# Kernel optimization log

Measured on AMD Instinct MI355X. Metric: run time of the kernel, lower is better.

The kernel has to match this reference:

```python
import jax, jax.numpy as jnp
import numpy as np

N = 100000      # nodes
E = 1600000     # edges (before self-loops)
IN_C = 128
HID = 256
L = 4
EPS = 1e-5


def setup_inputs() -> dict:
    key = jax.random.key(0)
    ks = jax.random.split(key, 12)
    s = 0.05
    x = jax.random.normal(ks[0], (N, IN_C), dtype=jnp.float32)
    edge_index = jax.random.randint(ks[1], (2, E), 0, N, dtype=jnp.int64)
    enc_w = jax.random.normal(ks[2], (IN_C, HID), dtype=jnp.float32) * s
    enc_b = jnp.zeros((HID,), jnp.float32)
    conv_w = jax.random.normal(ks[3], (L, HID, HID), dtype=jnp.float32) * s
    conv_b = jnp.zeros((L, HID), jnp.float32)
    ln_g = jnp.ones((L, HID), jnp.float32)
    ln_b = jnp.zeros((L, HID), jnp.float32)
    lin1_w = jax.random.normal(ks[4], (HID, HID // 2), dtype=jnp.float32) * s
    lin1_b = jnp.zeros((HID // 2,), jnp.float32)
    lin2_w = jax.random.normal(ks[5], (HID // 2, 1), dtype=jnp.float32) * s
    lin2_b = jnp.zeros((1,), jnp.float32)
    return dict(x=x, edge_index=edge_index, enc_w=enc_w, enc_b=enc_b,
                conv_w=conv_w, conv_b=conv_b, ln_g=ln_g, ln_b=ln_b,
                lin1_w=lin1_w, lin1_b=lin1_b, lin2_w=lin2_w, lin2_b=lin2_b)


def _layer_norm(h, g, b):
    mu = jnp.mean(h, axis=-1, keepdims=True)
    var = jnp.mean(jnp.square(h - mu), axis=-1, keepdims=True)
    return (h - mu) * jax.lax.rsqrt(var + EPS) * g + b


def reference(x, edge_index, enc_w, enc_b, conv_w, conv_b, ln_g, ln_b,
              lin1_w, lin1_b, lin2_w, lin2_b):
    loops = jnp.arange(N, dtype=edge_index.dtype)
    row = jnp.concatenate([edge_index[0], loops])   # source
    col = jnp.concatenate([edge_index[1], loops])   # target
    # GCN symmetric norm with self-loop weight 1 (improved=False)
    deg = jax.ops.segment_sum(jnp.ones(row.shape[0], jnp.float32), col,
                              num_segments=N)
    dis = jnp.where(deg > 0, jax.lax.rsqrt(deg), 0.0)  # deg^-1/2, [N]

    h = x @ enc_w + enc_b
    for i in range(L):
        hw = h @ conv_w[i]
        # norm_e = dis[row]*dis[col]: scale at source, aggregate, scale at target
        agg = jax.ops.segment_sum((hw * dis[:, None])[row], col,
                                  num_segments=N)
        h = agg * dis[:, None] + conv_b[i]
        h = jax.nn.relu(_layer_norm(h, ln_g[i], ln_b[i]))
        # dropout p=0.1 is identity in eval mode
    h = jax.nn.relu(h @ lin1_w + lin1_b)
    return h @ lin2_w + lin2_b  # [N, 1]
```

## Files before the change

### kernel.cpp

```cpp
#include <hip/hip_runtime.h>

#define N_NODES 100000
#define N_EDGES 1600000
#define IN_C    128
#define HID     256
#define NLAYER  4

#define NBUCK 391
#define BCAP  8192
#define EPB   4096
#define CAPL  6144

typedef __attribute__((ext_vector_type(8))) __bf16 bf16x8;
typedef __attribute__((ext_vector_type(4))) float  floatx4;
typedef __attribute__((ext_vector_type(2))) float  floatx2;

__device__ inline unsigned short f2b(float f) {
    unsigned u = __builtin_bit_cast(unsigned, f);
    return (unsigned short)((u + 0x7fffu + ((u >> 16) & 1u)) >> 16);
}
__device__ inline void acc8p(floatx2* a, uint4 v) {
    unsigned wds[4] = {v.x, v.y, v.z, v.w};
    #pragma unroll
    for (int k = 0; k < 4; ++k) {
        floatx2 t;
        t.x = __builtin_bit_cast(float, wds[k] << 16);
        t.y = __builtin_bit_cast(float, wds[k] & 0xffff0000u);
        a[k] += t;
    }
}

__global__ void kb_zero(int* g, int m) {
    int i = blockIdx.x * blockDim.x + threadIdx.x;
    if (i < m) g[i] = 0;
}

__global__ __launch_bounds__(256) void kb_scatter(
        const int* __restrict__ row, const int* __restrict__ col,
        int* __restrict__ gfill, uint2* __restrict__ pairs, int e) {
    __shared__ uint2 ep[EPB];
    __shared__ int hist[NBUCK];
    __shared__ int lbase[NBUCK];
    const int tid  = threadIdx.x;
    const int base = blockIdx.x * EPB;
    for (int b = tid; b < NBUCK; b += 256) hist[b] = 0;
    __syncthreads();
    #pragma unroll
    for (int k = 0; k < EPB / 256; ++k) {
        int i = base + k * 256 + tid;
        uint2 pr = make_uint2(0xffffffffu, 0u);
        if (i < e) {
            pr.x = (unsigned)col[i];
            pr.y = (unsigned)row[i];
            atomicAdd(&hist[pr.x >> 8], 1);
        }
        ep[k * 256 + tid] = pr;
    }
    __syncthreads();
    for (int b = tid; b < NBUCK; b += 256) {
        int h = hist[b];
        lbase[b] = h ? atomicAdd(&gfill[b], h) : 0;
    }
    __syncthreads();
    for (int b = tid; b < NBUCK; b += 256) hist[b] = 0;
    __syncthreads();
    #pragma unroll
    for (int k = 0; k < EPB / 256; ++k) {
        uint2 pr = ep[k * 256 + tid];
        if (pr.x != 0xffffffffu) {
            int bk = pr.x >> 8;
            int p  = lbase[bk] + atomicAdd(&hist[bk], 1);
            if (p < BCAP) pairs[(size_t)bk * BCAP + p] = pr;
        }
    }
}

__global__ void kb_scan(const int* __restrict__ gfill, int* __restrict__ boff,
                        int* __restrict__ offs) {
    __shared__ int wsum[8];
    const int t = threadIdx.x, lane = t & 63, w = t >> 6;
    int v = (t < NBUCK) ? gfill[t] : 0;
    int inc = v;
    #pragma unroll
    for (int o = 1; o < 64; o <<= 1) { int u = __shfl_up(inc, o); if (lane >= o) inc += u; }
    if (lane == 63) wsum[w] = inc;
    __syncthreads();
    if (t == 0) { int r = 0; for (int i = 0; i < 8; ++i) { int x = wsum[i]; wsum[i] = r; r += x; } }
    __syncthreads();
    int excl = wsum[w] + inc - v;
    if (t <= NBUCK) boff[t] = excl;
    if (t == 0) offs[N_NODES] = N_EDGES;
}

__global__ __launch_bounds__(256) void kb_build(
        const uint2* __restrict__ pairs, const int* __restrict__ gfill,
        const int* __restrict__ boff,
        int* __restrict__ offs, float* __restrict__ dis,
        int* __restrict__ srcl, int n) {
    __shared__ int lcnt[256];
    __shared__ int lstart[256];
    __shared__ int wsum[4];
    __shared__ int sl[CAPL];
    const int b = blockIdx.x;
    const int tid = threadIdx.x, lane = tid & 63, w = tid >> 6;
    int cnt = gfill[b]; if (cnt > CAPL) cnt = CAPL;
    const int base = boff[b];
    const uint2* bp = pairs + (size_t)b * BCAP;
    lcnt[tid] = 0;
    __syncthreads();
    for (int i = tid; i < cnt; i += 256)
        atomicAdd(&lcnt[bp[i].x & 255], 1);
    __syncthreads();
    int v = lcnt[tid];
    int inc = v;
    #pragma unroll
    for (int o = 1; o < 64; o <<= 1) { int u = __shfl_up(inc, o); if (lane >= o) inc += u; }
    if (lane == 63) wsum[w] = inc;
    __syncthreads();
    if (tid == 0) { int r = 0; for (int i = 0; i < 4; ++i) { int x = wsum[i]; wsum[i] = r; r += x; } }
    __syncthreads();
    int excl = wsum[w] + inc - v;
    lstart[tid] = excl;
    int node = (b << 8) + tid;
    if (node < n) {
        dis[node]  = rsqrtf((float)(v + 1));
        offs[node] = base + excl;
    }
    __syncthreads();
    lcnt[tid] = 0;
    __syncthreads();
    for (int i = tid; i < cnt; i += 256) {
        uint2 pr = bp[i];
        int c = pr.x & 255;
        int q = lstart[c] + atomicAdd(&lcnt[c], 1);
        sl[q] = (int)pr.y;
    }
    __syncthreads();
    for (int i = tid; i < cnt; i += 256)
        srcl[base + i] = sl[i];
}

__global__ void k_wt_all(const float* __restrict__ enc_w, const float* __restrict__ conv_w,
                         const float* __restrict__ w1,
                         unsigned short* __restrict__ enc_t, unsigned short* __restrict__ conv_t,
                         unsigned short* __restrict__ lin1_t) {
    int idx = blockIdx.x * blockDim.x + threadIdx.x;
    if (idx < IN_C * HID) {
        int k = idx / HID, n = idx % HID;
        enc_t[n * IN_C + k] = f2b(enc_w[idx]);
    } else if (idx < IN_C * HID + NLAYER * HID * HID) {
        int r = idx - IN_C * HID;
        int l = r / (HID * HID);
        int e = r % (HID * HID);
        int k = e / HID, n = e % HID;
        conv_t[(size_t)l * HID * HID + n * HID + k] = f2b(conv_w[r]);
    } else if (idx < IN_C * HID + NLAYER * HID * HID + HID * (HID / 2)) {
        int e = idx - (IN_C * HID + NLAYER * HID * HID);
        int k = e / (HID / 2), n = e % (HID / 2);
        lin1_t[n * HID + k] = f2b(w1[e]);
    }
}

template<int MODE>
__global__ __launch_bounds__(256) void k_mm(
        const void* __restrict__ Ain,
        const unsigned short* __restrict__ Wt,
        const float* __restrict__ bias, const float* __restrict__ scale,
        void* __restrict__ Cout, int M, int K, int Nn) {
    __shared__ unsigned short As[128 * 32];
    __shared__ unsigned short Bs[128 * 32];
    const int tid  = threadIdx.x;
    const int lane = tid & 63;
    const int w    = tid >> 6;
    const int bm   = blockIdx.x * 128;
    const int bn   = blockIdx.y * 128;

    const int i0 = tid, i1 = tid + 256;
    const int r0 = i0 >> 2, r1 = i1 >> 2;
    const int q0 = i0 & 3,  q1 = i1 & 3;
    const int a_off0 = min(bm + r0, M - 1) * K + q0 * 8;
    const int a_off1 = min(bm + r1, M - 1) * K + q1 * 8;
    const int b_off0 = (bn + r0) * K + q0 * 8;
    const int b_off1 = (bn + r1) * K + q1 * 8;

    floatx4 acc[4][4];
    #pragma unroll
    for (int i = 0; i < 4; ++i)
        #pragma unroll
        for (int j = 0; j < 4; ++j)
            acc[i][j] = (floatx4){0.f, 0.f, 0.f, 0.f};

    const int wm = (w & 1) * 64;
    const int wn = (w >> 1) * 64;
    const int fm = lane & 15;
    const int fq = (lane >> 4) * 8;

    const unsigned short* Ab = (const unsigned short*)Ain;
    const float*          Af = (const float*)Ain;

    uint4 ra0, ra1, rb0, rb1;
    auto loadA = [&](int koff, uint4& oa0, uint4& oa1) {
        if (MODE == 0) {
            float4 f0 = *(const float4*)(Af + a_off0 + koff);
            float4 f1 = *(const float4*)(Af + a_off0 + koff + 4);
            oa0.x = (unsigned)f2b(f0.x) | ((unsigned)f2b(f0.y) << 16);
            oa0.y = (unsigned)f2b(f0.z) | ((unsigned)f2b(f0.w) << 16);
            oa0.z = (unsigned)f2b(f1.x) | ((unsigned)f2b(f1.y) << 16);
            oa0.w = (unsigned)f2b(f1.z) | ((unsigned)f2b(f1.w) << 16);
            float4 g0 = *(const float4*)(Af + a_off1 + koff);
            float4 g1 = *(const float4*)(Af + a_off1 + koff + 4);
            oa1.x = (unsigned)f2b(g0.x) | ((unsigned)f2b(g0.y) << 16);
            oa1.y = (unsigned)f2b(g0.z) | ((unsigned)f2b(g0.w) << 16);
            oa1.z = (unsigned)f2b(g1.x) | ((unsigned)f2b(g1.y) << 16);
            oa1.w = (unsigned)f2b(g1.z) | ((unsigned)f2b(g1.w) << 16);
        } else {
            oa0 = *(const uint4*)(Ab + a_off0 + koff);
            oa1 = *(const uint4*)(Ab + a_off1 + koff);
        }
    };

    loadA(0, ra0, ra1);
    rb0 = *(const uint4*)(Wt + b_off0);
    rb1 = *(const uint4*)(Wt + b_off1);

    const int KT = K >> 5;
    for (int kt = 0; kt < KT; ++kt) {
        ((uint4*)As)[i0] = ra0; ((uint4*)As)[i1] = ra1;
        ((uint4*)Bs)[i0] = rb0; ((uint4*)Bs)[i1] = rb1;
        __syncthreads();
        if (kt + 1 < KT) {
            int k0 = (kt + 1) << 5;
            loadA(k0, ra0, ra1);
            rb0 = *(const uint4*)(Wt + b_off0 + k0);
            rb1 = *(const uint4*)(Wt + b_off1 + k0);
        }
        bf16x8 af[4], bfr[4];
        #pragma unroll
        for (int i = 0; i < 4; ++i)
            af[i] = *(const bf16x8*)(const void*)(As + (wm + i * 16 + fm) * 32 + fq);
        #pragma unroll
        for (int j = 0; j < 4; ++j)
            bfr[j] = *(const bf16x8*)(const void*)(Bs + (wn + j * 16 + fm) * 32 + fq);
        #pragma unroll
        for (int i = 0; i < 4; ++i)
            #pragma unroll
            for (int j = 0; j < 4; ++j)
                acc[i][j] = __builtin_amdgcn_mfma_f32_16x16x32_bf16(af[i], bfr[j], acc[i][j], 0, 0, 0);
        __syncthreads();
    }

    const int quad = lane >> 4;
    #pragma unroll
    for (int i = 0; i < 4; ++i) {
        #pragma unroll
        for (int r = 0; r < 4; ++r) {
            int row = bm + wm + i * 16 + quad * 4 + r;
            if (row >= M) continue;
            float sc = scale ? scale[row] : 1.f;
            #pragma unroll
            for (int j = 0; j < 4; ++j) {
                int colg = bn + wn + j * 16 + fm;
                float v = acc[i][j][r];
                if (MODE == 0) v += bias[colg];
                v *= sc;
                ((unsigned short*)Cout)[(size_t)row * Nn + colg] = f2b(v);
            }
        }
    }
}

__global__ __launch_bounds__(256) void k_head(
        const unsigned short* __restrict__ A,
        const unsigned short* __restrict__ Wt,
        const float* __restrict__ b1, const float* __restrict__ w2,
        const float* __restrict__ b2, float* __restrict__ out, int M) {
    const int K = 256;
    __shared__ unsigned short As[128 * 32];
    __shared__ unsigned short Bs[128 * 32];
    const int tid  = threadIdx.x;
    const int lane = tid & 63;
    const int w    = tid >> 6;
    const int bm   = blockIdx.x * 128;

    const int i0 = tid, i1 = tid + 256;
    const int r0 = i0 >> 2, r1 = i1 >> 2;
    const int q0 = i0 & 3,  q1 = i1 & 3;
    const int a_off0 = min(bm + r0, M - 1) * K + q0 * 8;
    const int a_off1 = min(bm + r1, M - 1) * K + q1 * 8;
    const int b_off0 = r0 * K + q0 * 8;
    const int b_off1 = r1 * K + q1 * 8;

    uint4 ra0, ra1, rb0, rb1;
    floatx4 acc[4][4];
    #pragma unroll
    for (int i = 0; i < 4; ++i)
        #pragma unroll
        for (int j = 0; j < 4; ++j)
            acc[i][j] = (floatx4){0.f, 0.f, 0.f, 0.f};

    const int wm = (w & 1) * 64;
    const int wn = (w >> 1) * 64;
    const int fm = lane & 15;
    const int fq = (lane >> 4) * 8;

    ra0 = *(const uint4*)(A + a_off0);
    ra1 = *(const uint4*)(A + a_off1);
    rb0 = *(const uint4*)(Wt + b_off0);
    rb1 = *(const uint4*)(Wt + b_off1);

    for (int kt = 0; kt < 8; ++kt) {
        ((uint4*)As)[i0] = ra0; ((uint4*)As)[i1] = ra1;
        ((uint4*)Bs)[i0] = rb0; ((uint4*)Bs)[i1] = rb1;
        __syncthreads();
        if (kt + 1 < 8) {
            int k0 = (kt + 1) << 5;
            ra0 = *(const uint4*)(A + a_off0 + k0);
            ra1 = *(const uint4*)(A + a_off1 + k0);
            rb0 = *(const uint4*)(Wt + b_off0 + k0);
            rb1 = *(const uint4*)(Wt + b_off1 + k0);
        }
        bf16x8 af[4], bfr[4];
        #pragma unroll
        for (int i = 0; i < 4; ++i)
            af[i] = *(const bf16x8*)(const void*)(As + (wm + i * 16 + fm) * 32 + fq);
        #pragma unroll
        for (int j = 0; j < 4; ++j)
            bfr[j] = *(const bf16x8*)(const void*)(Bs + (wn + j * 16 + fm) * 32 + fq);
        #pragma unroll
        for (int i = 0; i < 4; ++i)
            #pragma unroll
            for (int j = 0; j < 4; ++j)
                acc[i][j] = __builtin_amdgcn_mfma_f32_16x16x32_bf16(af[i], bfr[j], acc[i][j], 0, 0, 0);
        __syncthreads();
    }

    float* red = (float*)As;
    const int q = lane >> 4;
    float b1v[4], w2v[4];
    #pragma unroll
    for (int j = 0; j < 4; ++j) {
        int col = wn + j * 16 + fm;
        b1v[j] = b1[col]; w2v[j] = w2[col];
    }
    #pragma unroll
    for (int i = 0; i < 4; ++i) {
        #pragma unroll
        for (int r = 0; r < 4; ++r) {
            float s = 0.f;
            #pragma unroll
            for (int j = 0; j < 4; ++j)
                s += fmaxf(acc[i][j][r] + b1v[j], 0.f) * w2v[j];
            #pragma unroll
            for (int off = 1; off < 16; off <<= 1) s += __shfl_xor(s, off);
            if (fm == 0) {
                int m = wm + i * 16 + q * 4 + r;
                red[m * 2 + (wn >> 6)] = s;
            }
        }
    }
    __syncthreads();
    if (tid < 128) {
        int row = bm + tid;
        if (row < M) out[row] = red[tid * 2] + red[tid * 2 + 1] + b2[0];
    }
}

__global__ void k_agg(const unsigned short* __restrict__ hw, const int* __restrict__ srcl,
                      const int* __restrict__ offs, const float* __restrict__ dis,
                      const float* __restrict__ cb, const float* __restrict__ g,
                      const float* __restrict__ bt, unsigned short* __restrict__ hout, int n) {
    int gtid = blockIdx.x * blockDim.x + threadIdx.x;
    int node = __builtin_amdgcn_readfirstlane(gtid >> 6);
    int lane = threadIdx.x & 63;
    const int half = lane >> 5;
    const int sub  = lane & 31;
    const uint4* T = (const uint4*)hw;

    floatx2 A0[4], C0[4];
    #pragma unroll
    for (int k = 0; k < 4; ++k) { A0[k] = (floatx2){0.f, 0.f}; C0[k] = (floatx2){0.f, 0.f}; }
    if (half == 0) {
        uint4 v = T[(size_t)node * 32 + sub];
        acc8p(A0, v);
    }
    int p = offs[node], pe = offs[node + 1];
    for (; p + 15 < pe; p += 16) {
        int s[16];
        #pragma unroll
        for (int t = 0; t < 16; ++t) s[t] = srcl[p + t];
        uint4 v0 = T[(size_t)(half ? s[1]  : s[0])  * 32 + sub];
        uint4 v1 = T[(size_t)(half ? s[3]  : s[2])  * 32 + sub];
        uint4 v2 = T[(size_t)(half ? s[5]  : s[4])  * 32 + sub];
        uint4 v3 = T[(size_t)(half ? s[7]  : s[6])  * 32 + sub];
        uint4 v4 = T[(size_t)(half ? s[9]  : s[8])  * 32 + sub];
        uint4 v5 = T[(size_t)(half ? s[11] : s[10]) * 32 + sub];
        uint4 v6 = T[(size_t)(half ? s[13] : s[12]) * 32 + sub];
        uint4 v7 = T[(size_t)(half ? s[15] : s[14]) * 32 + sub];
        acc8p(A0, v0); acc8p(C0, v1); acc8p(A0, v2); acc8p(C0, v3);
        acc8p(A0, v4); acc8p(C0, v5); acc8p(A0, v6); acc8p(C0, v7);
    }
    for (; p + 7 < pe; p += 8) {
        int s0 = srcl[p],     s1 = srcl[p + 1], s2 = srcl[p + 2], s3 = srcl[p + 3];
        int s4 = srcl[p + 4], s5 = srcl[p + 5], s6 = srcl[p + 6], s7 = srcl[p + 7];
        uint4 v0 = T[(size_t)(half ? s1 : s0) * 32 + sub];
        uint4 v1 = T[(size_t)(half ? s3 : s2) * 32 + sub];
        uint4 v2 = T[(size_t)(half ? s5 : s4) * 32 + sub];
        uint4 v3 = T[(size_t)(half ? s7 : s6) * 32 + sub];
        acc8p(A0, v0); acc8p(C0, v1); acc8p(A0, v2); acc8p(C0, v3);
    }
    for (; p + 1 < pe; p += 2) {
        int s0 = srcl[p], s1 = srcl[p + 1];
        uint4 v = T[(size_t)(half ? s1 : s0) * 32 + sub];
        acc8p(A0, v);
    }
    if (p < pe && half == 0) {
        uint4 v = T[(size_t)srcl[p] * 32 + sub];
        acc8p(A0, v);
    }
    float a[8];
    #pragma unroll
    for (int k = 0; k < 4; ++k) {
        floatx2 t = A0[k] + C0[k];
        a[2 * k]     = t.x + __shfl_xor(t.x, 32);
        a[2 * k + 1] = t.y + __shfl_xor(t.y, 32);
    }
    float dc = dis[node];
    const float4* cb4 = (const float4*)cb;
    const float4* g4  = (const float4*)g;
    const float4* bt4 = (const float4*)bt;
    float4 cba = cb4[sub * 2], cbb = cb4[sub * 2 + 1];
    float h[8];
    h[0] = fmaf(a[0], dc, cba.x); h[1] = fmaf(a[1], dc, cba.y);
    h[2] = fmaf(a[2], dc, cba.z); h[3] = fmaf(a[3], dc, cba.w);
    h[4] = fmaf(a[4], dc, cbb.x); h[5] = fmaf(a[5], dc, cbb.y);
    h[6] = fmaf(a[6], dc, cbb.z); h[7] = fmaf(a[7], dc, cbb.w);
    float s = 0.f, sq = 0.f;
    #pragma unroll
    for (int j = 0; j < 8; ++j) { s += h[j]; sq += h[j] * h[j]; }
    #pragma unroll
    for (int off = 1; off < 32; off <<= 1) { s += __shfl_xor(s, off); sq += __shfl_xor(sq, off); }
    float mu  = s * (1.f / 256.f);
    float var = sq * (1.f / 256.f) - mu * mu;
    float inv = rsqrtf(var + 1e-5f);
    if (half == 0) {
        float4 ga = g4[sub * 2], gb = g4[sub * 2 + 1];
        float4 ba = bt4[sub * 2], bb = bt4[sub * 2 + 1];
        float gv[8] = {ga.x, ga.y, ga.z, ga.w, gb.x, gb.y, gb.z, gb.w};
        float bv[8] = {ba.x, ba.y, ba.z, ba.w, bb.x, bb.y, bb.z, bb.w};
        unsigned short o[8];
        #pragma unroll
        for (int j = 0; j < 8; ++j)
            o[j] = f2b(fmaxf(fmaf((h[j] - mu) * inv, gv[j], bv[j]), 0.f));
        uint4 st;
        st.x = (unsigned)o[0] | ((unsigned)o[1] << 16);
        st.y = (unsigned)o[2] | ((unsigned)o[3] << 16);
        st.z = (unsigned)o[4] | ((unsigned)o[5] << 16);
        st.w = (unsigned)o[6] | ((unsigned)o[7] << 16);
        ((uint4*)hout)[(size_t)node * 32 + sub] = st;
    }
}

extern "C" void kernel_launch(void* const* d_in, const int* in_sizes, int n_in,
                              void* d_out, int out_size, void* d_ws, size_t ws_size,
                              hipStream_t stream) {
    const float* x      = (const float*)d_in[0];
    const int*   ei     = (const int*)d_in[1];
    const float* enc_w  = (const float*)d_in[2];
    const float* enc_b  = (const float*)d_in[3];
    const float* conv_w = (const float*)d_in[4];
    const float* conv_b = (const float*)d_in[5];
    const float* ln_g   = (const float*)d_in[6];
    const float* ln_b   = (const float*)d_in[7];
    const float* w1     = (const float*)d_in[8];
    const float* b1     = (const float*)d_in[9];
    const float* w2     = (const float*)d_in[10];
    const float* b2     = (const float*)d_in[11];
    float* out = (float*)d_out;

    char* ws = (char*)d_ws;
    size_t off = 0;
    auto alloc = [&](size_t bytes) -> void* {
        void* p = ws + off;
        off = (off + bytes + 255) & ~(size_t)255;
        return p;
    };
    int*   offs  = (int*)alloc((size_t)(N_NODES + 1) * 4);
    int*   srcl  = (int*)alloc((size_t)N_EDGES * 4);
    float* dis   = (float*)alloc((size_t)N_NODES * 4);
    int*   gfill = (int*)alloc((size_t)NBUCK * 4);
    int*   boff  = (int*)alloc((size_t)(NBUCK + 1) * 4);
    unsigned short* hb = (unsigned short*)alloc((size_t)N_NODES * HID * 2);
    unsigned short* hw = (unsigned short*)alloc((size_t)N_NODES * HID * 2);
    uint2* pairs = (uint2*)alloc((size_t)NBUCK * BCAP * 8);
    unsigned short* enc_t  = (unsigned short*)alloc((size_t)IN_C * HID * 2);
    unsigned short* conv_t = (unsigned short*)alloc((size_t)NLAYER * HID * HID * 2);
    unsigned short* lin1_t = (unsigned short*)alloc((size_t)HID * (HID / 2) * 2);

    const int* row = ei;
    const int* col = ei + N_EDGES;

    kb_zero<<<(NBUCK + 255) / 256, 256, 0, stream>>>(gfill, NBUCK);
    kb_scatter<<<(N_EDGES + EPB - 1) / EPB, 256, 0, stream>>>(row, col, gfill, pairs, N_EDGES);
    kb_scan<<<1, 512, 0, stream>>>(gfill, boff, offs);
    kb_build<<<NBUCK, 256, 0, stream>>>(pairs, gfill, boff, offs, dis, srcl, N_NODES);

    {
        int tot = IN_C * HID + NLAYER * HID * HID + HID * (HID / 2);
        k_wt_all<<<(tot + 255) / 256, 256, 0, stream>>>(enc_w, conv_w, w1, enc_t, conv_t, lin1_t);
    }

    {
        dim3 g((N_NODES + 127) / 128, HID / 128);
        k_mm<0><<<g, 256, 0, stream>>>(x, enc_t, enc_b, nullptr, hb, N_NODES, IN_C, HID);
    }

    for (int l = 0; l < NLAYER; ++l) {
        dim3 g((N_NODES + 127) / 128, HID / 128);
        k_mm<1><<<g, 256, 0, stream>>>(hb, conv_t + (size_t)l * HID * HID, nullptr, dis,
                                       hw, N_NODES, HID, HID);
        k_agg<<<(N_NODES * 64 + 255) / 256, 256, 0, stream>>>(
            hw, srcl, offs, dis, conv_b + l * HID, ln_g + l * HID, ln_b + l * HID, hb, N_NODES);
    }

    k_head<<<(N_NODES + 127) / 128, 256, 0, stream>>>(hb, lin1_t, b1, w2, b2, out, N_NODES);
}
```

Measured before the change: 827.2 us.

## Slice hidden features into 16-column planes for cache-resident gather aggregation

The GEMM epilogue now writes hw into 16 column-sliced planes (N x 16 each, 3.2MB per plane), so each gather pass works on a table small enough to stay in L2. The new gather kernel processes one slice per block group with 8 edge slots per node and writes partial aggregates in bf16. A separate finalize kernel then applies the degree scaling, bias, layernorm and relu. This trades random full-row reads over a 51MB table for more cache-friendly per-slice gathers, but adds an extra intermediate round trip through memory, extra bf16 rounding of the aggregate, and one more launch per layer.

```diff
diff --git a/kernel.cpp b/kernel.cpp
--- a/kernel.cpp
+++ b/kernel.cpp
@@ -10,6 +10,8 @@
 #define BCAP  8192
 #define EPB   4096
 #define CAPL  6144
+
+#define NC    1600
 
 typedef __attribute__((ext_vector_type(8))) __bf16 bf16x8;
 typedef __attribute__((ext_vector_type(4))) float  floatx4;
@@ -259,11 +261,16 @@
             float sc = scale ? scale[row] : 1.f;
             #pragma unroll
             for (int j = 0; j < 4; ++j) {
-                int colg = bn + wn + j * 16 + fm;
                 float v = acc[i][j][r];
-                if (MODE == 0) v += bias[colg];
-                v *= sc;
-                ((unsigned short*)Cout)[(size_t)row * Nn + colg] = f2b(v);
+                if (MODE == 0) {
+                    int colg = bn + wn + j * 16 + fm;
+                    v = (v + bias[colg]) * sc;
+                    ((unsigned short*)Cout)[(size_t)row * Nn + colg] = f2b(v);
+                } else {
+                    v *= sc;
+                    int region = ((bn + wn) >> 4) + j;
+                    ((unsigned short*)Cout)[(size_t)region * N_NODES * 16 + (size_t)row * 16 + fm] = f2b(v);
+                }
             }
         }
     }
@@ -365,99 +372,101 @@
     }
 }
 
-__global__ void k_agg(const unsigned short* __restrict__ hw, const int* __restrict__ srcl,
-                      const int* __restrict__ offs, const float* __restrict__ dis,
+__global__ __launch_bounds__(256) void k_gat(
+        const unsigned short* __restrict__ Ts,
+        const int* __restrict__ srcl, const int* __restrict__ offs,
+        unsigned short* __restrict__ agg) {
+    const int GC = (N_NODES + NC - 1) / NC;
+    int b = blockIdx.x;
+    int B2 = 8 * GC;
+    int phase = (b >= B2) ? 1 : 0;
+    int r = b - phase * B2;
+    int slice = ((r & 7) << 1) | phase;
+    int chunk = r >> 3;
+    const unsigned short* T = Ts  + (size_t)slice * N_NODES * 16;
+    unsigned short*       A = agg + (size_t)slice * N_NODES * 16;
+    const int lane = threadIdx.x & 63;
+    const int w    = threadIdx.x >> 6;
+    const int grp  = lane >> 4;
+    const int t    = lane & 15;
+    const int half = t & 1;
+    const int slot = t >> 1;
+    const int baseW = chunk * NC + w * (NC / 4);
+
+    for (int rnd = 0; rnd < NC / 16; ++rnd) {
+        int node = baseW + rnd * 4 + grp;
+        bool valid = node < N_NODES;
+        floatx2 acc[4];
+        #pragma unroll
+        for (int k = 0; k < 4; ++k) acc[k] = (floatx2){0.f, 0.f};
+        if (valid) {
+            int ps = offs[node];
+            int items = offs[node + 1] - ps + 1;
+            int i = slot;
+            if (i < items) {
+                int src = (i == 0) ? node : srcl[ps + i - 1];
+                while (true) {
+                    int ni = i + 8;
+                    int nsrc = (ni < items) ? srcl[ps + ni - 1] : 0;
+                    uint4 v = *(const uint4*)(T + (size_t)src * 16 + half * 8);
+                    acc8p(acc, v);
+                    if (ni >= items) break;
+                    i = ni; src = nsrc;
+                }
+            }
+        }
+        #pragma unroll
+        for (int k = 0; k < 4; ++k) {
+            floatx2 v = acc[k];
+            v.x += __shfl_xor(v.x, 2); v.y += __shfl_xor(v.y, 2);
+            v.x += __shfl_xor(v.x, 4); v.y += __shfl_xor(v.y, 4);
+            v.x += __shfl_xor(v.x, 8); v.y += __shfl_xor(v.y, 8);
+            acc[k] = v;
+        }
+        if (slot == 0 && valid) {
+            uint4 st;
+            st.x = (unsigned)f2b(acc[0].x) | ((unsigned)f2b(acc[0].y) << 16);
+            st.y = (unsigned)f2b(acc[1].x) | ((unsigned)f2b(acc[1].y) << 16);
+            st.z = (unsigned)f2b(acc[2].x) | ((unsigned)f2b(acc[2].y) << 16);
+            st.w = (unsigned)f2b(acc[3].x) | ((unsigned)f2b(acc[3].y) << 16);
+            *(uint4*)(A + (size_t)node * 16 + half * 8) = st;
+        }
+    }
+}
+
+__global__ void k_fin(const unsigned short* __restrict__ agg,
+                      const float* __restrict__ dis,
                       const float* __restrict__ cb, const float* __restrict__ g,
-                      const float* __restrict__ bt, unsigned short* __restrict__ hout, int n) {
+                      const float* __restrict__ bt,
+                      unsigned short* __restrict__ hout, int n) {
     int gtid = blockIdx.x * blockDim.x + threadIdx.x;
-    int node = __builtin_amdgcn_readfirstlane(gtid >> 6);
+    int node = gtid >> 6;
     int lane = threadIdx.x & 63;
-    const int half = lane >> 5;
-    const int sub  = lane & 31;
-    const uint4* T = (const uint4*)hw;
-
-    floatx2 A0[4], C0[4];
-    #pragma unroll
-    for (int k = 0; k < 4; ++k) { A0[k] = (floatx2){0.f, 0.f}; C0[k] = (floatx2){0.f, 0.f}; }
-    if (half == 0) {
-        uint4 v = T[(size_t)node * 32 + sub];
-        acc8p(A0, v);
-    }
-    int p = offs[node], pe = offs[node + 1];
-    for (; p + 15 < pe; p += 16) {
-        int s[16];
-        #pragma unroll
-        for (int t = 0; t < 16; ++t) s[t] = srcl[p + t];
-        uint4 v0 = T[(size_t)(half ? s[1]  : s[0])  * 32 + sub];
-        uint4 v1 = T[(size_t)(half ? s[3]  : s[2])  * 32 + sub];
-        uint4 v2 = T[(size_t)(half ? s[5]  : s[4])  * 32 + sub];
-        uint4 v3 = T[(size_t)(half ? s[7]  : s[6])  * 32 + sub];
-        uint4 v4 = T[(size_t)(half ? s[9]  : s[8])  * 32 + sub];
-        uint4 v5 = T[(size_t)(half ? s[11] : s[10]) * 32 + sub];
-        uint4 v6 = T[(size_t)(half ? s[13] : s[12]) * 32 + sub];
-        uint4 v7 = T[(size_t)(half ? s[15] : s[14]) * 32 + sub];
-        acc8p(A0, v0); acc8p(C0, v1); acc8p(A0, v2); acc8p(C0, v3);
-        acc8p(A0, v4); acc8p(C0, v5); acc8p(A0, v6); acc8p(C0, v7);
-    }
-    for (; p + 7 < pe; p += 8) {
-        int s0 = srcl[p],     s1 = srcl[p + 1], s2 = srcl[p + 2], s3 = srcl[p + 3];
-        int s4 = srcl[p + 4], s5 = srcl[p + 5], s6 = srcl[p + 6], s7 = srcl[p + 7];
-        uint4 v0 = T[(size_t)(half ? s1 : s0) * 32 + sub];
-        uint4 v1 = T[(size_t)(half ? s3 : s2) * 32 + sub];
-        uint4 v2 = T[(size_t)(half ? s5 : s4) * 32 + sub];
-        uint4 v3 = T[(size_t)(half ? s7 : s6) * 32 + sub];
-        acc8p(A0, v0); acc8p(C0, v1); acc8p(A0, v2); acc8p(C0, v3);
-    }
-    for (; p + 1 < pe; p += 2) {
-        int s0 = srcl[p], s1 = srcl[p + 1];
-        uint4 v = T[(size_t)(half ? s1 : s0) * 32 + sub];
-        acc8p(A0, v);
-    }
-    if (p < pe && half == 0) {
-        uint4 v = T[(size_t)srcl[p] * 32 + sub];
-        acc8p(A0, v);
-    }
-    float a[8];
-    #pragma unroll
-    for (int k = 0; k < 4; ++k) {
-        floatx2 t = A0[k] + C0[k];
-        a[2 * k]     = t.x + __shfl_xor(t.x, 32);
-        a[2 * k + 1] = t.y + __shfl_xor(t.y, 32);
-    }
+    if (node >= n) return;
+    int s = lane >> 2;
+    int o = (lane & 3) * 4;
+    uint2 v = *(const uint2*)(agg + (size_t)s * N_NODES * 16 + (size_t)node * 16 + o);
     float dc = dis[node];
-    const float4* cb4 = (const float4*)cb;
-    const float4* g4  = (const float4*)g;
-    const float4* bt4 = (const float4*)bt;
-    float4 cba = cb4[sub * 2], cbb = cb4[sub * 2 + 1];
-    float h[8];
-    h[0] = fmaf(a[0], dc, cba.x); h[1] = fmaf(a[1], dc, cba.y);
-    h[2] = fmaf(a[2], dc, cba.z); h[3] = fmaf(a[3], dc, cba.w);
-    h[4] = fmaf(a[4], dc, cbb.x); h[5] = fmaf(a[5], dc, cbb.y);
-    h[6] = fmaf(a[6], dc, cbb.z); h[7] = fmaf(a[7], dc, cbb.w);
-    float s = 0.f, sq = 0.f;
-    #pragma unroll
-    for (int j = 0; j < 8; ++j) { s += h[j]; sq += h[j] * h[j]; }
-    #pragma unroll
-    for (int off = 1; off < 32; off <<= 1) { s += __shfl_xor(s, off); sq += __shfl_xor(sq, off); }
-    float mu  = s * (1.f / 256.f);
+    float4 cbv = ((const float4*)cb)[lane];
+    float h0 = fmaf(__builtin_bit_cast(float, v.x << 16),          dc, cbv.x);
+    float h1 = fmaf(__builtin_bit_cast(float, v.x & 0xffff0000u),  dc, cbv.y);
+    float h2 = fmaf(__builtin_bit_cast(float, v.y << 16),          dc, cbv.z);
+    float h3 = fmaf(__builtin_bit_cast(float, v.y & 0xffff0000u),  dc, cbv.w);
+    float sm = h0 + h1 + h2 + h3;
+    float sq = h0 * h0 + h1 * h1 + h2 * h2 + h3 * h3;
+    #pragma unroll
+    for (int off = 1; off < 64; off <<= 1) { sm += __shfl_xor(sm, off); sq += __shfl_xor(sq, off); }
+    float mu  = sm * (1.f / 256.f);
     float var = sq * (1.f / 256.f) - mu * mu;
     float inv = rsqrtf(var + 1e-5f);
-    if (half == 0) {
-        float4 ga = g4[sub * 2], gb = g4[sub * 2 + 1];
-        float4 ba = bt4[sub * 2], bb = bt4[sub * 2 + 1];
-        float gv[8] = {ga.x, ga.y, ga.z, ga.w, gb.x, gb.y, gb.z, gb.w};
-        float bv[8] = {ba.x, ba.y, ba.z, ba.w, bb.x, bb.y, bb.z, bb.w};
-        unsigned short o[8];
-        #pragma unroll
-        for (int j = 0; j < 8; ++j)
-            o[j] = f2b(fmaxf(fmaf((h[j] - mu) * inv, gv[j], bv[j]), 0.f));
-        uint4 st;
-        st.x = (unsigned)o[0] | ((unsigned)o[1] << 16);
-        st.y = (unsigned)o[2] | ((unsigned)o[3] << 16);
-        st.z = (unsigned)o[4] | ((unsigned)o[5] << 16);
-        st.w = (unsigned)o[6] | ((unsigned)o[7] << 16);
-        ((uint4*)hout)[(size_t)node * 32 + sub] = st;
-    }
+    float4 gv = ((const float4*)g)[lane];
+    float4 bv = ((const float4*)bt)[lane];
+    ushort4 ot;
+    ot.x = f2b(fmaxf(fmaf((h0 - mu) * inv, gv.x, bv.x), 0.f));
+    ot.y = f2b(fmaxf(fmaf((h1 - mu) * inv, gv.y, bv.y), 0.f));
+    ot.z = f2b(fmaxf(fmaf((h2 - mu) * inv, gv.z, bv.z), 0.f));
+    ot.w = f2b(fmaxf(fmaf((h3 - mu) * inv, gv.w, bv.w), 0.f));
+    *(ushort4*)(hout + (size_t)node * 256 + lane * 4) = ot;
 }
 
 extern "C" void kernel_launch(void* const* d_in, const int* in_sizes, int n_in,
@@ -491,7 +500,11 @@
     int*   boff  = (int*)alloc((size_t)(NBUCK + 1) * 4);
     unsigned short* hb = (unsigned short*)alloc((size_t)N_NODES * HID * 2);
     unsigned short* hw = (unsigned short*)alloc((size_t)N_NODES * HID * 2);
-    uint2* pairs = (uint2*)alloc((size_t)NBUCK * BCAP * 8);
+    size_t pairs_bytes = (size_t)NBUCK * BCAP * 8;
+    size_t agg_bytes   = (size_t)N_NODES * HID * 2;
+    char* OV = (char*)alloc(pairs_bytes > agg_bytes ? pairs_bytes : agg_bytes);
+    uint2*          pairs = (uint2*)OV;
+    unsigned short* agg   = (unsigned short*)OV;
     unsigned short* enc_t  = (unsigned short*)alloc((size_t)IN_C * HID * 2);
     unsigned short* conv_t = (unsigned short*)alloc((size_t)NLAYER * HID * HID * 2);
     unsigned short* lin1_t = (unsigned short*)alloc((size_t)HID * (HID / 2) * 2);
@@ -514,12 +527,14 @@
         k_mm<0><<<g, 256, 0, stream>>>(x, enc_t, enc_b, nullptr, hb, N_NODES, IN_C, HID);
     }
 
+    const int GC = (N_NODES + NC - 1) / NC;
     for (int l = 0; l < NLAYER; ++l) {
         dim3 g((N_NODES + 127) / 128, HID / 128);
         k_mm<1><<<g, 256, 0, stream>>>(hb, conv_t + (size_t)l * HID * HID, nullptr, dis,
                                        hw, N_NODES, HID, HID);
-        k_agg<<<(N_NODES * 64 + 255) / 256, 256, 0, stream>>>(
-            hw, srcl, offs, dis, conv_b + l * HID, ln_g + l * HID, ln_b + l * HID, hb, N_NODES);
+        k_gat<<<16 * GC, 256, 0, stream>>>(hw, srcl, offs, agg);
+        k_fin<<<(N_NODES * 64) / 256, 256, 0, stream>>>(
+            agg, dis, conv_b + l * HID, ln_g + l * HID, ln_b + l * HID, hb, N_NODES);
     }
 
     k_head<<<(N_NODES + 127) / 128, 256, 0, stream>>>(hb, lin1_t, b1, w2, b2, out, N_NODES);
```

New measurement: 1.526 ms. 84.5% more time.
